# Performance work log

Hardware: AMD Instinct MI355X
Metric: run time of the kernel (lower is better)

The kernel has to match this reference:

```python
import jax, jax.numpy as jnp
import numpy as np

B, S, H, NH = 1, 2048, 768, 12
HD = H // NH  # 64


def setup_inputs() -> dict:
    key = jax.random.key(0)
    k0, k1, k2, k3 = jax.random.split(key, 4)
    BN = B * S
    return {
        "hidden_states": jax.random.normal(k0, (B, S, H), dtype=jnp.float32),
        "g": jax.random.uniform(k1, (BN, BN), dtype=jnp.float32),
        "attention_mask": jnp.zeros((B, S), dtype=jnp.float32),
        "Wq": jax.random.normal(k2, (H, H), dtype=jnp.float32) * 0.02,
        "bq": jnp.zeros((H,), dtype=jnp.float32),
        "Wv": jax.random.normal(k3, (H, H), dtype=jnp.float32) * 0.02,
        "bv": jnp.zeros((H,), dtype=jnp.float32),
    }


def reference(hidden_states, g, attention_mask, Wq, bq, Wv, bv):
    # hidden_states: [B, S, H] -> torch code transposes to [S, B, H]
    hs = jnp.swapaxes(hidden_states, 0, 1)  # [S, B, H]
    s, b, h = hs.shape
    BN = s * b

    q = hs @ Wq.T + bq  # [S, B, H]
    v = hs @ Wv.T + bv  # [S, B, H]

    # view(S,B,NH,HD).transpose(0,1) -> [B,S,NH,HD], then flat reshape to [NH, BN, HD]
    q = jnp.swapaxes(q.reshape(s, b, NH, HD), 0, 1).reshape(NH, BN, HD)
    # L2-normalize each query vector along head_dim (torch F.normalize, eps=1e-12)
    q = q / jnp.maximum(jnp.linalg.norm(q, axis=2, keepdims=True), 1e-12)

    # value: [B,S,NH,HD] flattened to [BN, NH, HD]
    v = jnp.swapaxes(v.reshape(s, b, NH, HD), 0, 1).reshape(BN, NH, HD)

    # attn sparsification mask combine (computed in original, but never used downstream)
    bool_mask = (attention_mask >= 0).reshape(-1, 1).astype(g.dtype)  # [BN, 1]
    _g_masked = g * (bool_mask @ bool_mask.T)  # dead value, kept for faithfulness

    # L2-distance attention scores: -(AA - 2AB + BB) / sqrt(head_dim)
    AB = jnp.einsum('hnd,hmd->hnm', q, q)            # [NH, BN, BN]
    AA = jnp.sum(q * q, axis=-1, keepdims=True)      # [NH, BN, 1]
    sim = -(AA - 2.0 * AB + jnp.swapaxes(AA, -1, -2)) * (HD ** -0.5)
    attn = jax.nn.softmax(sim, axis=-1)              # [NH, BN, BN]

    # weighted value sum: bmm(attn, v.transpose(0,1)) -> [NH, BN, HD]
    out = jnp.einsum('hnm,hmd->hnd', attn, jnp.swapaxes(v, 0, 1))

    # reshape(B,S,NH,HD) then merge last two dims -> [B, S, H]
    out = out.reshape(b, s, NH, HD).reshape(b, s, h)
    return out
```

## Files before the change

### kernel.cpp

```cpp
#include <hip/hip_runtime.h>
#include <math.h>

#define NTOK 2048
#define HDIM 768
#define NHEAD 12
#define NQ (NTOK * NHEAD)

typedef __attribute__((ext_vector_type(8))) short short8v;
typedef __attribute__((ext_vector_type(4))) float float4v;

static __device__ __forceinline__ unsigned short f2bf(float x) {
    unsigned u = __float_as_uint(x);
    return (unsigned short)((u + 0x7fffu + ((u >> 16) & 1u)) >> 16);
}
static __device__ __forceinline__ unsigned pk2(float a, float b) {
    unsigned r;
    asm("v_cvt_pk_bf16_f32 %0, %1, %2" : "=v"(r) : "v"(a), "v"(b));
    return r;
}
static __device__ __forceinline__ void gload_lds16(const void* g, void* lds_uniform) {
    __builtin_amdgcn_global_load_lds(
        (const __attribute__((address_space(1))) void*)g,
        (__attribute__((address_space(3))) void*)lds_uniform, 16, 0, 0);
}

__global__ __launch_bounds__(256) void projnorm_kernel(
    const float* __restrict__ hs, const float* __restrict__ Wq,
    const float* __restrict__ bq, const float* __restrict__ Wv,
    const float* __restrict__ bv, unsigned short* __restrict__ qbf,
    unsigned short* __restrict__ vT)
{
    constexpr int PITCH = 40;
    __shared__ unsigned short As[2][128 * PITCH];
    __shared__ unsigned short Bs[2][64 * PITCH];

    const bool isq = (blockIdx.z == 0);
    const float* W    = isq ? Wq : Wv;
    const float* bias = isq ? bq : bv;
    const int n0 = blockIdx.x * 64, m0 = blockIdx.y * 128;
    const int tid = threadIdx.x, lane = tid & 63, w = tid >> 6;

    const int arow = tid >> 1, acol = (tid & 1) * 16;
    const int brow = tid >> 2, bcol = (tid & 3) * 8;
    const float* ag = hs + (size_t)(m0 + arow) * HDIM + acol;
    const float* bg = W + (size_t)(n0 + brow) * HDIM + bcol;

    float4 ga[4], gb[2];
#define PLOAD(k0)                                                              \
    {                                                                          \
        _Pragma("unroll") for (int i = 0; i < 4; ++i)                          \
            ga[i] = *(const float4*)(ag + (k0) + i * 4);                       \
        _Pragma("unroll") for (int i = 0; i < 2; ++i)                          \
            gb[i] = *(const float4*)(bg + (k0) + i * 4);                       \
    }
#define PCVTW(b)                                                               \
    {                                                                          \
        uint4 u0 = {pk2(ga[0].x, ga[0].y), pk2(ga[0].z, ga[0].w),              \
                    pk2(ga[1].x, ga[1].y), pk2(ga[1].z, ga[1].w)};             \
        uint4 u1 = {pk2(ga[2].x, ga[2].y), pk2(ga[2].z, ga[2].w),              \
                    pk2(ga[3].x, ga[3].y), pk2(ga[3].z, ga[3].w)};             \
        *(uint4*)&As[b][arow * PITCH + acol]     = u0;                         \
        *(uint4*)&As[b][arow * PITCH + acol + 8] = u1;                         \
        uint4 u2 = {pk2(gb[0].x, gb[0].y), pk2(gb[0].z, gb[0].w),              \
                    pk2(gb[1].x, gb[1].y), pk2(gb[1].z, gb[1].w)};             \
        *(uint4*)&Bs[b][brow * PITCH + bcol] = u2;                             \
    }

    float4v acc[2][4];
    #pragma unroll
    for (int fr = 0; fr < 2; ++fr)
        #pragma unroll
        for (int fc = 0; fc < 4; ++fc) acc[fr][fc] = (float4v){0.f, 0.f, 0.f, 0.f};

    PLOAD(0);
    PCVTW(0);

    for (int ks = 0; ks < 24; ++ks) {
        const int b = ks & 1;
        if (ks < 23) PLOAD((ks + 1) * 32);
        __syncthreads();
        short8v af[2], bf[4];
        #pragma unroll
        for (int fr = 0; fr < 2; ++fr)
            af[fr] = *(const short8v*)
                &As[b][(w * 32 + fr * 16 + (lane & 15)) * PITCH + ((lane >> 4) << 3)];
        #pragma unroll
        for (int fc = 0; fc < 4; ++fc)
            bf[fc] = *(const short8v*)
                &Bs[b][(fc * 16 + (lane & 15)) * PITCH + ((lane >> 4) << 3)];
        #pragma unroll
        for (int fr = 0; fr < 2; ++fr)
            #pragma unroll
            for (int fc = 0; fc < 4; ++fc)
                acc[fr][fc] = __builtin_amdgcn_mfma_f32_16x16x32_bf16(
                    af[fr], bf[fc], acc[fr][fc], 0, 0, 0);
        if (ks < 23) PCVTW(b ^ 1);
    }
#undef PLOAD
#undef PCVTW

    float bcol4[4];
    #pragma unroll
    for (int fc = 0; fc < 4; ++fc) bcol4[fc] = bias[n0 + fc * 16 + (lane & 15)];

    if (isq) {
        #pragma unroll
        for (int fr = 0; fr < 2; ++fr)
            #pragma unroll
            for (int r = 0; r < 4; ++r) {
                float v[4];
                float ss = 0.f;
                #pragma unroll
                for (int fc = 0; fc < 4; ++fc) {
                    v[fc] = acc[fr][fc][r] + bcol4[fc];
                    ss = fmaf(v[fc], v[fc], ss);
                }
                ss += __shfl_xor(ss, 1);
                ss += __shfl_xor(ss, 2);
                ss += __shfl_xor(ss, 4);
                ss += __shfl_xor(ss, 8);
                float inv = 1.0f / fmaxf(sqrtf(ss), 1e-12f);
                int m = m0 + w * 32 + fr * 16 + ((lane >> 4) << 2) + r;
                #pragma unroll
                for (int fc = 0; fc < 4; ++fc)
                    qbf[(size_t)m * HDIM + n0 + fc * 16 + (lane & 15)] = f2bf(v[fc] * inv);
            }
    } else {
        #pragma unroll
        for (int fr = 0; fr < 2; ++fr)
            #pragma unroll
            for (int fc = 0; fc < 4; ++fc) {
                int f = n0 + fc * 16 + (lane & 15);
                int mtk = m0 + w * 32 + fr * 16 + ((lane >> 4) << 2);
                union { unsigned short u[4]; unsigned long long q; } pk;
                #pragma unroll
                for (int r = 0; r < 4; ++r) pk.u[r] = f2bf(acc[fr][fc][r] + bcol4[fc]);
                *(unsigned long long*)(vT + (size_t)f * NTOK + mtk) = pk.q;
            }
    }
}

__global__ __launch_bounds__(128)
__attribute__((amdgpu_waves_per_eu(3, 3)))
void attn_kernel(
    const unsigned short* __restrict__ qbf,
    const unsigned short* __restrict__ vT,
    float* __restrict__ num0,
    float* __restrict__ part1,
    float* __restrict__ lbuf)
{
    __shared__ unsigned short Ksb[2][64 * 64];
    __shared__ unsigned short Pl[2][16 * 72];

    const int bid = blockIdx.x;
    const int swz = (bid & 7) * 192 + (bid >> 3);
    const int h = swz >> 7, rem = swz & 127;
    const int qt = rem >> 1, ksp = rem & 1;
    const int tid = threadIdx.x, lane = tid & 63, w = tid >> 6;
    const int n0 = qt * 32;
    const int kbase0 = ksp * 1024;

    const unsigned short* kh = qbf + (size_t)h * NTOK * 64;
    const unsigned short* vh = vT + (size_t)h * 64 * NTOK;

    const unsigned short* qrow = kh + ((size_t)n0 + w * 16 + (lane & 15)) * 64;
    short8v qa[2];
    qa[0] = *(const short8v*)(qrow + ((lane >> 4) << 3));
    qa[1] = *(const short8v*)(qrow + 32 + ((lane >> 4) << 3));

#define STAGE_K(buf, m0v)                                                      \
    {                                                                          \
        _Pragma("unroll")                                                      \
        for (int i = 0; i < 4; ++i) {           \
            int ci = ((w * 4 + i) << 6) + lane;                                \
            int r = ci >> 3, c8 = (ci & 7) ^ (r & 7);                          \
            gload_lds16(kh + ((size_t)(m0v) + r) * 64 + (c8 << 3),             \
                        (char*)&Ksb[buf][0] + ((w * 4 + i) << 10));            \
        }                                                                      \
    }
    short8v vfA[8], vfB[8];
#define LOADV(VF, mb)                                                          \
    _Pragma("unroll")                                                          \
    for (int t = 0; t < 4; ++t)                                                \
        _Pragma("unroll")                                                      \
        for (int kk = 0; kk < 2; ++kk)                                         \
            VF[t * 2 + kk] = *(const short8v*)(                                \
                vh + (size_t)(t * 16 + (lane & 15)) * NTOK + (mb) +            \
                kk * 32 + ((lane >> 4) << 3));

    float4v acc[4];
    #pragma unroll
    for (int t = 0; t < 4; ++t) acc[t] = (float4v){0.f, 0.f, 0.f, 0.f};
    float lsum = 0.f;

#define TILE_BODY(MT, KB, VFC, VFN, LAST)                                      \
    {                                                                          \
        if (!(LAST)) {                                                         \
            STAGE_K((KB) ^ 1, kbase0 + ((MT) + 1) * 64);                       \
            LOADV(VFN, kbase0 + ((MT) + 1) * 64);                              \
            __builtin_amdgcn_sched_barrier(0);            \
        }                                                                      \
                     \
        float4v St[4];                                                         \
        __builtin_amdgcn_s_setprio(1);                                         \
        _Pragma("unroll")                                                      \
        for (int t = 0; t < 4; ++t) {                                          \
            St[t] = (float4v){0.f, 0.f, 0.f, 0.f};                             \
            _Pragma("unroll")                                                  \
            for (int kk = 0; kk < 2; ++kk) {                                   \
                int row = (lane & 15) + (t << 4);                              \
                int off = ((row << 7) + (kk << 6) + ((lane >> 4) << 4)) ^      \
                          ((row & 7) << 4);                                    \
                short8v kf = *(const short8v*)((const char*)&Ksb[KB][0] + off);\
                St[t] = __builtin_amdgcn_mfma_f32_16x16x32_bf16(               \
                    kf, qa[kk], St[t], 0, 0, 0);                               \
            }                                                                  \
        }                                                                      \
        __builtin_amdgcn_s_setprio(0);                                         \
                     \
        float p[4][4];                                                         \
        float ls = 0.f;                                                        \
        _Pragma("unroll")                                                      \
        for (int t = 0; t < 4; ++t)                                            \
            _Pragma("unroll")                                                  \
            for (int r = 0; r < 4; ++r) {                                      \
                p[t][r] = __expf(St[t][r] * 0.25f);                            \
                ls += p[t][r];                                                 \
            }                                                                  \
        ls += __shfl_xor(ls, 16);                                              \
        ls += __shfl_xor(ls, 32);                                              \
        lsum += ls;                                                            \
                         \
        _Pragma("unroll")                                                      \
        for (int t = 0; t < 4; ++t) {                                          \
            unsigned w0 = pk2(p[t][0], p[t][1]);                               \
            unsigned w1 = pk2(p[t][2], p[t][3]);                               \
            unsigned long long q64 =                                           \
                (unsigned long long)w0 | ((unsigned long long)w1 << 32);       \
            *(unsigned long long*)(&Pl[w][(lane & 15) * 72 + t * 16 +          \
                                          ((lane >> 4) << 2)]) = q64;          \
        }                                                                      \
        asm volatile("s_waitcnt lgkmcnt(0)" ::: "memory");                     \
        __builtin_amdgcn_sched_barrier(0);                                     \
        short8v pf[2];                                                         \
        _Pragma("unroll")                                                      \
        for (int kk = 0; kk < 2; ++kk)                                         \
            pf[kk] = *(const short8v*)(&Pl[w][(lane & 15) * 72 + kk * 32 +     \
                                              ((lane >> 4) << 3)]);            \
         \
        __builtin_amdgcn_s_setprio(1);                                         \
        _Pragma("unroll")                                                      \
        for (int t = 0; t < 4; ++t) {                                          \
            acc[t] = __builtin_amdgcn_mfma_f32_16x16x32_bf16(                  \
                pf[0], VFC[t * 2 + 0], acc[t], 0, 0, 0);                       \
            acc[t] = __builtin_amdgcn_mfma_f32_16x16x32_bf16(                  \
                pf[1], VFC[t * 2 + 1], acc[t], 0, 0, 0);                       \
        }                                                                      \
        __builtin_amdgcn_s_setprio(0);                                         \
        if (!(LAST)) {                                                         \
            asm volatile("s_waitcnt vmcnt(8)" ::: "memory");   \
            __builtin_amdgcn_s_barrier();                  \
            __builtin_amdgcn_sched_barrier(0);                                 \
        }                                                                      \
    }

    STAGE_K(0, kbase0);
    LOADV(vfA, kbase0);
    __syncthreads();

    for (int it = 0; it < 8; ++it) {
        TILE_BODY(2 * it,     0, vfA, vfB, false);
        if (it < 7) {
            TILE_BODY(2 * it + 1, 1, vfB, vfA, false);
        } else {
            TILE_BODY(2 * it + 1, 1, vfB, vfA, true);
        }
    }
#undef TILE_BODY
#undef STAGE_K
#undef LOADV

    float* nout = ksp ? part1 : num0;
    #pragma unroll
    for (int r = 0; r < 4; ++r) {
        int n = n0 + w * 16 + ((lane >> 4) << 2) + r;
        #pragma unroll
        for (int t = 0; t < 4; ++t)
            nout[((size_t)h * NTOK + n) * 64 + t * 16 + (lane & 15)] = acc[t][r];
    }
    if (lane < 16)
        lbuf[ksp * NQ + h * NTOK + n0 + w * 16 + lane] = lsum;
}

__global__ __launch_bounds__(256) void combine_kernel(
    float* __restrict__ out, const float* __restrict__ part1,
    const float* __restrict__ lbuf)
{
    int gid = blockIdx.x * 256 + threadIdx.x;
    float4 a = ((const float4*)out)[gid];
    float4 b = ((const float4*)part1)[gid];
    int row = gid >> 4;
    float inv = 1.0f / (lbuf[row] + lbuf[NQ + row]);
    float4 o;
    o.x = (a.x + b.x) * inv; o.y = (a.y + b.y) * inv;
    o.z = (a.z + b.z) * inv; o.w = (a.w + b.w) * inv;
    ((float4*)out)[gid] = o;
}

extern "C" void kernel_launch(void* const* d_in, const int* in_sizes, int n_in,
                              void* d_out, int out_size, void* d_ws, size_t ws_size,
                              hipStream_t stream)
{
    const float* hs = (const float*)d_in[0];
    const float* Wq = (const float*)d_in[3];
    const float* bq = (const float*)d_in[4];
    const float* Wv = (const float*)d_in[5];
    const float* bv = (const float*)d_in[6];
    float* out = (float*)d_out;

    unsigned short* qbf   = (unsigned short*)d_ws;
    unsigned short* vT    = qbf + (size_t)NTOK * HDIM;
    float*          part1 = (float*)(vT + (size_t)HDIM * NTOK);
    float*          lbuf  = part1 + (size_t)NQ * 64;

    projnorm_kernel<<<dim3(12, 16, 2), 256, 0, stream>>>(
        hs, Wq, bq, Wv, bv, qbf, vT);
    attn_kernel<<<dim3(1536), 128, 0, stream>>>(qbf, vT, out, part1, lbuf);
    combine_kernel<<<dim3(1536), 256, 0, stream>>>(out, part1, lbuf);
}
```

Before: 153.9 us.

## Load K tiles directly into registers instead of staging through LDS

The attention kernel no longer copies K tiles into shared memory with global_load_lds and swizzled reads. Each wave now loads its K fragments straight from global memory into double-buffered registers, the same way V is loaded. This drops the per-tile workgroup barrier and the LDS traffic. In exchange each of the two waves fetches the full K tile separately, so global traffic for K roughly doubles, and register use rises, which is why occupancy is cut from 3 to 2 waves per EU.

```diff
diff --git a/kernel.cpp b/kernel.cpp
--- a/kernel.cpp
+++ b/kernel.cpp
@@ -17,11 +17,6 @@
     unsigned r;
     asm("v_cvt_pk_bf16_f32 %0, %1, %2" : "=v"(r) : "v"(a), "v"(b));
     return r;
-}
-static __device__ __forceinline__ void gload_lds16(const void* g, void* lds_uniform) {
-    __builtin_amdgcn_global_load_lds(
-        (const __attribute__((address_space(1))) void*)g,
-        (__attribute__((address_space(3))) void*)lds_uniform, 16, 0, 0);
 }
 
 __global__ __launch_bounds__(256) void projnorm_kernel(
@@ -141,7 +136,7 @@
 }
 
 __global__ __launch_bounds__(128)
-__attribute__((amdgpu_waves_per_eu(3, 3)))
+__attribute__((amdgpu_waves_per_eu(2, 2)))
 void attn_kernel(
     const unsigned short* __restrict__ qbf,
     const unsigned short* __restrict__ vT,
@@ -149,7 +144,6 @@
     float* __restrict__ part1,
     float* __restrict__ lbuf)
 {
-    __shared__ unsigned short Ksb[2][64 * 64];
     __shared__ unsigned short Pl[2][16 * 72];
 
     const int bid = blockIdx.x;
@@ -168,17 +162,15 @@
     qa[0] = *(const short8v*)(qrow + ((lane >> 4) << 3));
     qa[1] = *(const short8v*)(qrow + 32 + ((lane >> 4) << 3));
 
-#define STAGE_K(buf, m0v)                                                      \
-    {                                                                          \
-        _Pragma("unroll")                                                      \
-        for (int i = 0; i < 4; ++i) {           \
-            int ci = ((w * 4 + i) << 6) + lane;                                \
-            int r = ci >> 3, c8 = (ci & 7) ^ (r & 7);                          \
-            gload_lds16(kh + ((size_t)(m0v) + r) * 64 + (c8 << 3),             \
-                        (char*)&Ksb[buf][0] + ((w * 4 + i) << 10));            \
-        }                                                                      \
-    }
-    short8v vfA[8], vfB[8];
+    short8v kfA[8], kfB[8], vfA[8], vfB[8];
+#define LOADK(KF, mb)                                                          \
+    _Pragma("unroll")                                                          \
+    for (int t = 0; t < 4; ++t)                                                \
+        _Pragma("unroll")                                                      \
+        for (int kk = 0; kk < 2; ++kk)                                         \
+            KF[t * 2 + kk] = *(const short8v*)(                                \
+                kh + ((size_t)((mb) + t * 16 + (lane & 15))) * 64 +            \
+                kk * 32 + ((lane >> 4) << 3));
 #define LOADV(VF, mb)                                                          \
     _Pragma("unroll")                                                          \
     for (int t = 0; t < 4; ++t)                                                \
@@ -193,10 +185,10 @@
     for (int t = 0; t < 4; ++t) acc[t] = (float4v){0.f, 0.f, 0.f, 0.f};
     float lsum = 0.f;
 
-#define TILE_BODY(MT, KB, VFC, VFN, LAST)                                      \
+#define TILE_BODY(MT, KFC, KFN, VFC, VFN, LAST)                                \
     {                                                                          \
         if (!(LAST)) {                                                         \
-            STAGE_K((KB) ^ 1, kbase0 + ((MT) + 1) * 64);                       \
+            LOADK(KFN, kbase0 + ((MT) + 1) * 64);                              \
             LOADV(VFN, kbase0 + ((MT) + 1) * 64);                              \
             __builtin_amdgcn_sched_barrier(0);            \
         }                                                                      \
@@ -206,15 +198,10 @@
         _Pragma("unroll")                                                      \
         for (int t = 0; t < 4; ++t) {                                          \
             St[t] = (float4v){0.f, 0.f, 0.f, 0.f};                             \
-            _Pragma("unroll")                                                  \
-            for (int kk = 0; kk < 2; ++kk) {                                   \
-                int row = (lane & 15) + (t << 4);                              \
-                int off = ((row << 7) + (kk << 6) + ((lane >> 4) << 4)) ^      \
-                          ((row & 7) << 4);                                    \
-                short8v kf = *(const short8v*)((const char*)&Ksb[KB][0] + off);\
-                St[t] = __builtin_amdgcn_mfma_f32_16x16x32_bf16(               \
-                    kf, qa[kk], St[t], 0, 0, 0);                               \
-            }                                                                  \
+            St[t] = __builtin_amdgcn_mfma_f32_16x16x32_bf16(                   \
+                KFC[t * 2 + 0], qa[0], St[t], 0, 0, 0);                        \
+            St[t] = __builtin_amdgcn_mfma_f32_16x16x32_bf16(                   \
+                KFC[t * 2 + 1], qa[1], St[t], 0, 0, 0);                        \
         }                                                                      \
         __builtin_amdgcn_s_setprio(0);                                         \
                      \
@@ -247,7 +234,7 @@
         for (int kk = 0; kk < 2; ++kk)                                         \
             pf[kk] = *(const short8v*)(&Pl[w][(lane & 15) * 72 + kk * 32 +     \
                                               ((lane >> 4) << 3)]);            \
-         \
+                                                             \
         __builtin_amdgcn_s_setprio(1);                                         \
         _Pragma("unroll")                                                      \
         for (int t = 0; t < 4; ++t) {                                          \
@@ -257,27 +244,21 @@
                 pf[1], VFC[t * 2 + 1], acc[t], 0, 0, 0);                       \
         }                                                                      \
         __builtin_amdgcn_s_setprio(0);                                         \
-        if (!(LAST)) {                                                         \
-            asm volatile("s_waitcnt vmcnt(8)" ::: "memory");   \
-            __builtin_amdgcn_s_barrier();                  \
-            __builtin_amdgcn_sched_barrier(0);                                 \
-        }                                                                      \
-    }
-
-    STAGE_K(0, kbase0);
+    }
+
+    LOADK(kfA, kbase0);
     LOADV(vfA, kbase0);
-    __syncthreads();
 
     for (int it = 0; it < 8; ++it) {
-        TILE_BODY(2 * it,     0, vfA, vfB, false);
+        TILE_BODY(2 * it,     kfA, kfB, vfA, vfB, false);
         if (it < 7) {
-            TILE_BODY(2 * it + 1, 1, vfB, vfA, false);
+            TILE_BODY(2 * it + 1, kfB, kfA, vfB, vfA, false);
         } else {
-            TILE_BODY(2 * it + 1, 1, vfB, vfA, true);
+            TILE_BODY(2 * it + 1, kfB, kfA, vfB, vfA, true);
         }
     }
 #undef TILE_BODY
-#undef STAGE_K
+#undef LOADK
 #undef LOADV
 
     float* nout = ksp ? part1 : num0;
```

Result: slower. 186.2 us (+21.0%).
